# Optimization experiments

Hardware: AMD Instinct MI355X
Metric: run time of the kernel (lower is better)

The kernel has to match this reference:

```python
import jax, jax.numpy as jnp
import numpy as np

B, L, T, F, H, O = 4096, 50, 64, 3, 20, 16

def setup_inputs() -> dict:
    key = jax.random.key(0)
    ks = jax.random.split(key, 20)
    p = lambda k, s: jax.random.normal(k, s, jnp.float32) * 0.1
    inp = {
        'x': jax.random.normal(ks[0], (B, L, T, F), jnp.float32),
        'lengths': jax.random.randint(ks[1], (B, L), 0, T, jnp.int32),
        # LSTMCell params (torch gate order i,f,g,o)
        'w_ih': p(ks[2], (4 * H, F)), 'w_hh': p(ks[3], (4 * H, H)),
        'b_ih': p(ks[4], (4 * H,)), 'b_hh': p(ks[5], (4 * H,)),
        # layer-summary Linear(20,16)
        'w_lin': p(ks[6], (O, H)), 'b_lin': p(ks[7], (O,)),
        # ClassifyNet convs
        'c1_w': p(ks[8], (32, 16, 5)), 'c1_b': p(ks[9], (32,)),
        'c2_w': p(ks[10], (32, 32, 4)), 'c2_b': p(ks[11], (32,)),
        'c3_w': p(ks[12], (32, 32, 4)), 'c3_b': p(ks[13], (32,)),
        'fc1_w': p(ks[14], (16, 32 * 19)), 'fc1_b': p(ks[15], (16,)),
        'fc2_w': p(ks[16], (4, 16)), 'fc2_b': p(ks[17], (4,)),
    }
    return inp

def _conv1d(x, w, b, stride):
    y = jax.lax.conv_general_dilated(x, w, (stride,), 'VALID',
                                     dimension_numbers=('NCH', 'OIH', 'NCH'))
    return y + b[None, :, None]

def _lstm_last_h(xseq, lens, w_ih, w_hh, b_ih, b_hh):
    # xseq: [N,T,F] padded; lens: [N]. Masked batched LSTM, returns h at step len-1.
    N = xseq.shape[0]
    xT = jnp.swapaxes(xseq, 0, 1)  # [T,N,F]
    h0 = jnp.zeros((N, H), xseq.dtype)
    def step(carry, inp):
        h, c = carry
        x_t, t = inp
        gates = x_t @ w_ih.T + b_ih + h @ w_hh.T + b_hh
        i, f, g, o = jnp.split(gates, 4, axis=-1)
        c_new = jax.nn.sigmoid(f) * c + jax.nn.sigmoid(i) * jnp.tanh(g)
        h_new = jax.nn.sigmoid(o) * jnp.tanh(c_new)
        m = (t < lens)[:, None]
        return (jnp.where(m, h_new, h), jnp.where(m, c_new, c)), None
    (h, _), _ = jax.lax.scan(step, (h0, h0), (xT, jnp.arange(xT.shape[0])))
    return h

def reference(x, lengths, w_ih, w_hh, b_ih, b_hh, w_lin, b_lin,
              c1_w, c1_b, c2_w, c2_b, c3_w, c3_b, fc1_w, fc1_b, fc2_w, fc2_b):
    N = B * L
    xf = x.reshape(N, T, F)
    lens = lengths.reshape(N)
    h = _lstm_last_h(xf, lens, w_ih, w_hh, b_ih, b_hh)          # [N,20]
    summ = jax.nn.sigmoid(h @ w_lin.T + b_lin)                   # [N,16]
    summ = jnp.where((lens > 0)[:, None], summ, 0.0)             # empty layer -> zeros
    feat = jnp.swapaxes(summ.reshape(B, L, O), 1, 2)             # [B,16,50]
    y = jax.nn.relu(_conv1d(feat, c1_w, c1_b, 1))                # [B,32,46]
    y = jax.nn.relu(_conv1d(y, c2_w, c2_b, 2))                   # [B,32,22]
    y = jax.nn.relu(_conv1d(y, c3_w, c3_b, 1))                   # [B,32,19]
    y = y.reshape(B, 32 * 19)
    y = jax.nn.relu(y @ fc1_w.T + fc1_b)
    return y @ fc2_w.T + fc2_b                                   # [B,4]
```

## Files before the change

kernel.cpp:

```cpp
#include <hip/hip_runtime.h>
#include <cstdint>
#include <cstddef>

#define NB 4096
#define NL 50
#define NT 64
#define NF 3
#define NH 20
#define NO 16
#define NN (NB*NL)
#define SB 16
#define WPB 2
#define TS 16
#define HSTR 20
#define XSTR 8

typedef __attribute__((ext_vector_type(8))) short bf16x8;
typedef __attribute__((ext_vector_type(4))) float f32x4;
typedef uint2 u2a __attribute__((may_alias));
typedef uint4 u4a __attribute__((may_alias));

#if defined(__has_builtin)
#  if __has_builtin(__builtin_amdgcn_exp2f)
#    define EXP2(x) __builtin_amdgcn_exp2f(x)
#  endif
#endif
#ifndef EXP2
extern "C" __device__ float __ocml_exp2_f32(float);
#  define EXP2(x) __ocml_exp2_f32(x)
#endif

__device__ __forceinline__ float fsig(float z) {
    return __builtin_amdgcn_rcpf(1.0f + __expf(-z));
}
__device__ __forceinline__ unsigned short f2bf(float f) {
    unsigned int x = __float_as_uint(f);
    x = (x + 0x7fffu + ((x >> 16) & 1u)) >> 16;
    return (unsigned short)x;
}
__device__ __forceinline__ float bf2f(unsigned short u) {
    return __uint_as_float(((unsigned int)u) << 16);
}
__device__ __forceinline__ unsigned int cvtpk(float a, float b) {
    unsigned int r;
    asm("v_cvt_pk_bf16_f32 %0, %1, %2" : "=v"(r) : "v"(a), "v"(b));
    return r;
}

__global__ __launch_bounds__(256) void hist_kernel(const int* __restrict__ lengths,
                                                   int* __restrict__ hist) {
    __shared__ int lh[64];
    int tid = threadIdx.x;
    if (tid < 64) lh[tid] = 0;
    __syncthreads();
    int n = blockIdx.x * 256 + tid;
    if (n < NN) {
        int len = lengths[n];
        len = len < 0 ? 0 : (len > 63 ? 63 : len);
        atomicAdd(&lh[len], 1);
    }
    __syncthreads();
    if (tid < 64 && lh[tid] != 0) atomicAdd(&hist[tid], lh[tid]);
}

__global__ __launch_bounds__(128) void prep_kernel(
    const int*   __restrict__ hist,
    int*         __restrict__ cursor,
    const float* __restrict__ w_hh,
    const float* __restrict__ b_ih,
    const float* __restrict__ b_hh,
    const float* __restrict__ w_ih,
    unsigned int* __restrict__ wfrag)
{
    int tid = threadIdx.x;
    if (tid < 64) {
        int l = tid;
        int v = hist[l];
        int s = v;
#pragma unroll
        for (int d = 1; d < 64; d <<= 1) {
            int o = __shfl_up(s, d);
            if (l >= d) s += o;
        }
        cursor[l] = s - v;
    } else {
        int l = tid - 64;
        int m = l & 15, kg = l >> 4;
        for (int T = 0; T < 5; ++T) {
            int g = (m & 3) * 20 + T * 4 + (m >> 2);
            int jt = g / 20;
            float sc = (jt == 2) ? 2.8853900817779268f : -1.4426950408889634f;
            unsigned int hi[4], lo[4];
            for (int d = 0; d < 4; ++d) {
                unsigned int hw[2], lw[2];
                for (int e = 0; e < 2; ++e) {
                    int k = kg * 8 + d * 2 + e;
                    float v = 0.0f;
                    if (k < 20)       v = w_hh[g * 20 + k];
                    else if (k <= 22) v = w_ih[g * 3 + (k - 20)];
                    else if (k == 23) v = b_ih[g] + b_hh[g];
                    else if (k <= 26) v = w_ih[g * 3 + (k - 24)];
                    v *= sc;
                    unsigned short h16 = f2bf(v);
                    float r = v - bf2f(h16);
                    hw[e] = h16; lw[e] = f2bf(r);
                }
                hi[d] = hw[0] | (hw[1] << 16);
                lo[d] = lw[0] | (lw[1] << 16);
            }
            for (int d = 0; d < 4; ++d) {
                wfrag[(size_t)((T * 2 + 0) * 64 + l) * 4 + d] = hi[d];
                wfrag[(size_t)((T * 2 + 1) * 64 + l) * 4 + d] = lo[d];
            }
        }
    }
}

__global__ __launch_bounds__(256) void scatter_kernel(const int* __restrict__ lengths,
                                                      int* __restrict__ cursor,
                                                      int* __restrict__ order,
                                                      int* __restrict__ len_s) {
    __shared__ int lcnt[64];
    __shared__ int lbase[64];
    int tid = threadIdx.x;
    if (tid < 64) lcnt[tid] = 0;
    __syncthreads();
    int n = blockIdx.x * 256 + tid;
    int len = 0, myrank = 0;
    if (n < NN) {
        len = lengths[n];
        len = len < 0 ? 0 : (len > 63 ? 63 : len);
        myrank = atomicAdd(&lcnt[len], 1);
    }
    __syncthreads();
    if (tid < 64 && lcnt[tid] != 0) lbase[tid] = atomicAdd(&cursor[tid], lcnt[tid]);
    __syncthreads();
    if (n < NN) {
        int pos = lbase[len] + myrank;
        order[pos] = n;
        len_s[pos] = len;
    }
}

#define LSTM_STEP(K, MASKED)                                                     \
    {                                                                            \
        uint2 ra_ = *(const u2a*)(p1 + (K) * st1);                               \
        uint2 rb_ = *(const u2a*)(p2 + (K) * st2);                               \
        union { uint4 u; bf16x8 v; } bb_;                                        \
        bb_.u = make_uint4(ra_.x, ra_.y, rb_.x, rb_.y);                          \
        f32x4 acc[5];                                                            \
        _Pragma("unroll")                                                        \
        for (int T = 0; T < 5; ++T) {                                            \
            f32x4 z4 = {0.f, 0.f, 0.f, 0.f};                                     \
            z4     = __builtin_amdgcn_mfma_f32_16x16x32_bf16(wf[2*T],   bb_.v, z4, 0, 0, 0); \
            acc[T] = __builtin_amdgcn_mfma_f32_16x16x32_bf16(wf[2*T+1], bb_.v, z4, 0, 0, 0); \
        }                                                                        \
        bool m_ = true;                                                          \
        if (MASKED) m_ = (t0 + (K)) < mylen;                                     \
        _Pragma("unroll")                                                        \
        for (int T = 0; T < 5; ++T) {                                            \
            float Ei = EXP2(acc[T][0]);                            \
            float Ef = EXP2(acc[T][1]);                            \
            float G  = EXP2(acc[T][2]);                           \
            float Eo = EXP2(acc[T][3]);                            \
            float Ai = 1.0f + Ei, Af = 1.0f + Ef, Bg = 1.0f + G;                 \
            float t1 = Ai * Bg;                                                  \
            float num = fmaf(G - 1.0f, Af, c5[T] * t1);                          \
            float cn  = num * __builtin_amdgcn_rcpf(t1 * Af);                    \
            float ce2 = fminf(cn * 2.8853900817779268f, 43.3f);                  \
            float Ec  = EXP2(ce2);                         \
            float hn  = (Ec - 1.0f) *                                            \
                        __builtin_amdgcn_rcpf((1.0f + Eo) * (1.0f + Ec));        \
        unsigned int hp_ = cvtpk(hn, hn);                                        \
        if (m_) {                                                                \
            c5[T] = cn;                                                          \
            hbf[wid][hoff + T * 4] = (unsigned short)hp_;                        \
        }                                                                        \
        }                                                                        \
    }

__global__ __launch_bounds__(128) void lstm_kernel(
    const float* __restrict__ x,
    const int*   __restrict__ len_s,
    const int*   __restrict__ order,
    const unsigned int* __restrict__ wfrag,
    const float* __restrict__ w_lin,
    const float* __restrict__ b_lin,
    float* __restrict__ feat)
{
    __shared__ __align__(16) unsigned short hbf[WPB][SB * HSTR];
    __shared__ __align__(16) unsigned short xbf[WPB][TS * SB * XSTR];
    __shared__ __align__(16) unsigned short zbuf[WPB][8];

    const int tid  = threadIdx.x;
    const int wid  = __builtin_amdgcn_readfirstlane(tid >> 6);
    const int lane = tid & 63;
    const int n16  = lane & 15;
    const int kg   = lane >> 4;
    const int base = ((gridDim.x - 1 - blockIdx.x) * WPB + wid) * SB;

    const int mylen   = len_s[base + n16];
    const int wavemin = len_s[base];
    const int wavemax = len_s[base + SB - 1];

    for (int i = lane; i < SB * HSTR; i += 64) hbf[wid][i] = 0;
    if (lane < 8) zbuf[wid][lane] = 0;

    bf16x8 wf[10];
#pragma unroll
    for (int p = 0; p < 10; ++p) {
        union { uint4 i; bf16x8 v; } cv;
        cv.i = ((const uint4*)wfrag)[p * 64 + lane];
        wf[p] = cv.v;
    }

    int nown = order[base + n16];
    const int ssl = lane >> 2;
    const int tq  = lane & 3;
    int nsl = __shfl(nown, ssl);
    const size_t gbase = (size_t)nsl * (NT * NF) + (size_t)tq * 12;

    const unsigned short* hpw = &hbf[wid][n16 * HSTR];
    const unsigned short* p1 = (kg < 3) ? (hpw + kg * 8)
                                        : &xbf[wid][n16 * XSTR + 4];
    const unsigned short* p2 = (kg < 2) ? (hpw + kg * 8 + 4)
                             : (kg == 2 ? &xbf[wid][n16 * XSTR]
                                        : &zbuf[wid][0]);
    const int st1 = (kg == 3) ? SB * XSTR : 0;
    const int st2 = (kg == 2) ? SB * XSTR : 0;
    const int hoff = n16 * HSTR + kg;

    float c5[5];
#pragma unroll
    for (int j = 0; j < 5; ++j) c5[j] = 0.0f;

    if (wavemax > 0) {
        float4 vf[3];
#pragma unroll
        for (int j = 0; j < 3; ++j) vf[j] = *(const float4*)(x + gbase + 4 * j);

        for (int t0 = 0; t0 < wavemax; t0 += TS) {
            float f12[12] = {vf[0].x, vf[0].y, vf[0].z, vf[0].w,
                             vf[1].x, vf[1].y, vf[1].z, vf[1].w,
                             vf[2].x, vf[2].y, vf[2].z, vf[2].w};
#pragma unroll
            for (int jj = 0; jj < 4; ++jj) {
                float a0 = f12[3 * jj], a1 = f12[3 * jj + 1], a2 = f12[3 * jj + 2];
                unsigned int w0 = cvtpk(a0, a1);
                unsigned int w1 = cvtpk(a2, 1.0f);
                float r0 = a0 - __uint_as_float(w0 << 16);
                float r1 = a1 - __uint_as_float(w0 & 0xFFFF0000u);
                float r2 = a2 - __uint_as_float(w1 << 16);
                unsigned int w2 = cvtpk(r0, r1);
                unsigned int w3 = cvtpk(r2, 0.0f);
                int t = tq * 4 + jj;
                *(u4a*)&xbf[wid][(t * SB + ssl) * XSTR] = make_uint4(w0, w1, w2, w3);
            }
            if (t0 + TS < wavemax) {
                size_t off = (size_t)(t0 + TS) * NF;
#pragma unroll
                for (int j = 0; j < 3; ++j)
                    vf[j] = *(const float4*)(x + gbase + off + 4 * j);
            }

            int kmax = wavemax - t0; if (kmax > TS) kmax = TS;
            int ku = wavemin - t0;
            ku = ku < 0 ? 0 : (ku > kmax ? kmax : ku);
            int k = 0;
            for (; k < ku; ++k)   LSTM_STEP(k, false)
            for (; k < kmax; ++k) LSTM_STEP(k, true)
        }
    }

    float hl[NH];
#pragma unroll
    for (int u = 0; u < NH; ++u) hl[u] = bf2f(hbf[wid][n16 * HSTR + u]);
    float4 res;
    if (mylen > 0) {
        float r4[4];
#pragma unroll
        for (int j = 0; j < 4; ++j) {
            int o = 4 * kg + j;
            float aa = b_lin[o];
#pragma unroll
            for (int kk = 0; kk < NH; ++kk) aa += w_lin[o * NH + kk] * hl[kk];
            r4[j] = fsig(aa);
        }
        res = make_float4(r4[0], r4[1], r4[2], r4[3]);
    } else {
        res = make_float4(0.f, 0.f, 0.f, 0.f);
    }
    *(float4*)(feat + (size_t)nown * NO + 4 * kg) = res;
}

__global__ __launch_bounds__(256) void head_kernel(
    const float* __restrict__ feat,
    const float* __restrict__ c1w, const float* __restrict__ c1b,
    const float* __restrict__ c2w, const float* __restrict__ c2b,
    const float* __restrict__ c3w, const float* __restrict__ c3b,
    const float* __restrict__ f1w, const float* __restrict__ f1b,
    const float* __restrict__ f2w, const float* __restrict__ f2b,
    float* __restrict__ out)
{
    const int b0  = blockIdx.x * 2;
    const int tid = threadIdx.x;
    const int p   = tid & 63;
    const int q   = __builtin_amdgcn_readfirstlane(tid >> 6);
    const int half = p >> 5;
    const int pp   = p & 31;

    __shared__ float sf[2][16 * 50];
    __shared__ float y1[2][32 * 46];
    __shared__ float y2[2][32 * 22];
    __shared__ __align__(16) float y3[2][32 * 19];
    __shared__ float r1[2][16];

    for (int i = tid; i < 2 * NL * NO; i += 256) {
        int bb = (i >= NL * NO) ? 1 : 0;
        int j = i - bb * (NL * NO);
        int l = j >> 4, o = j & 15;
        sf[bb][o * 50 + l] = feat[(size_t)(b0 + bb) * (NL * NO) + j];
    }
    __syncthreads();

    const int oc0 = q * 8;

#pragma unroll
    for (int bb = 0; bb < 2; ++bb) {
        if (p < 46) {
            float acc[8];
#pragma unroll
            for (int oc = 0; oc < 8; ++oc) acc[oc] = c1b[oc0 + oc];
#pragma unroll
            for (int ic = 0; ic < 16; ++ic) {
#pragma unroll
                for (int tap = 0; tap < 5; ++tap) {
                    float fv = sf[bb][ic * 50 + p + tap];
#pragma unroll
                    for (int oc = 0; oc < 8; ++oc)
                        acc[oc] += c1w[((oc0 + oc) * 16 + ic) * 5 + tap] * fv;
                }
            }
#pragma unroll
            for (int oc = 0; oc < 8; ++oc)
                y1[bb][(oc0 + oc) * 46 + p] = fmaxf(acc[oc], 0.0f);
        }
    }
    __syncthreads();

    if (pp < 22) {
        float acc[8];
#pragma unroll
        for (int oc = 0; oc < 8; ++oc) acc[oc] = c2b[oc0 + oc];
#pragma unroll
        for (int ic = 0; ic < 32; ++ic) {
#pragma unroll
            for (int tap = 0; tap < 4; ++tap) {
                float fv = y1[half][ic * 46 + 2 * pp + tap];
#pragma unroll
                for (int oc = 0; oc < 8; ++oc)
                    acc[oc] += c2w[((oc0 + oc) * 32 + ic) * 4 + tap] * fv;
            }
        }
#pragma unroll
        for (int oc = 0; oc < 8; ++oc)
            y2[half][(oc0 + oc) * 22 + pp] = fmaxf(acc[oc], 0.0f);
    }
    __syncthreads();

    if (pp < 19) {
        float acc[8];
#pragma unroll
        for (int oc = 0; oc < 8; ++oc) acc[oc] = c3b[oc0 + oc];
#pragma unroll
        for (int ic = 0; ic < 32; ++ic) {
#pragma unroll
            for (int tap = 0; tap < 4; ++tap) {
                float fv = y2[half][ic * 22 + pp + tap];
#pragma unroll
                for (int oc = 0; oc < 8; ++oc)
                    acc[oc] += c3w[((oc0 + oc) * 32 + ic) * 4 + tap] * fv;
            }
        }
#pragma unroll
        for (int oc = 0; oc < 8; ++oc)
            y3[half][(oc0 + oc) * 19 + pp] = fmaxf(acc[oc], 0.0f);
    }
    __syncthreads();

    if (q < 2) {
        int u  = p & 15;
        int qq = p >> 4;
        const float4* wv = (const float4*)(f1w + u * 608 + qq * 152);
        const float4* yv = (const float4*)(&y3[q][qq * 152]);
        float acc = 0.0f;
#pragma unroll 2
        for (int k = 0; k < 38; ++k) {
            float4 a = wv[k], bv = yv[k];
            acc += a.x * bv.x + a.y * bv.y + a.z * bv.z + a.w * bv.w;
        }
        acc += __shfl_xor(acc, 16);
        acc += __shfl_xor(acc, 32);
        if (p < 16) r1[q][p] = fmaxf(acc + f1b[p], 0.0f);
    }
    __syncthreads();

    if (q < 2 && p < 4) {
        float s = f2b[p];
#pragma unroll
        for (int k = 0; k < 16; ++k) s += f2w[p * 16 + k] * r1[q][k];
        out[(size_t)(b0 + q) * 4 + p] = s;
    }
}

extern "C" void kernel_launch(void* const* d_in, const int* in_sizes, int n_in,
                              void* d_out, int out_size, void* d_ws, size_t ws_size,
                              hipStream_t stream)
{
    const float* x     = (const float*)d_in[0];
    const int*  lengths= (const int*)  d_in[1];
    const float* w_ih  = (const float*)d_in[2];
    const float* w_hh  = (const float*)d_in[3];
    const float* b_ih  = (const float*)d_in[4];
    const float* b_hh  = (const float*)d_in[5];
    const float* w_lin = (const float*)d_in[6];
    const float* b_lin = (const float*)d_in[7];
    const float* c1w   = (const float*)d_in[8];
    const float* c1b   = (const float*)d_in[9];
    const float* c2w   = (const float*)d_in[10];
    const float* c2b   = (const float*)d_in[11];
    const float* c3w   = (const float*)d_in[12];
    const float* c3b   = (const float*)d_in[13];
    const float* f1w   = (const float*)d_in[14];
    const float* f1b   = (const float*)d_in[15];
    const float* f2w   = (const float*)d_in[16];
    const float* f2b   = (const float*)d_in[17];
    float* out = (float*)d_out;

    char* ws      = (char*)d_ws;
    float* feat   = (float*)ws;
    int*   order  = (int*)(feat + (size_t)NN * NO);
    int*   len_s  = order + NN;
    int*   hist   = len_s + NN;
    int*   cursor = hist + 64;
    unsigned int* wfrag = (unsigned int*)(cursor + 64);

    hipMemsetAsync(hist, 0, 64 * sizeof(int), stream);
    hist_kernel   <<<NN / 256, 256, 0, stream>>>(lengths, hist);
    prep_kernel   <<<1, 128, 0, stream>>>(hist, cursor, w_hh, b_ih, b_hh, w_ih, wfrag);
    scatter_kernel<<<NN / 256, 256, 0, stream>>>(lengths, cursor, order, len_s);
    lstm_kernel   <<<NN / (SB * WPB), 128, 0, stream>>>(x, len_s, order, wfrag,
                                                        w_lin, b_lin, feat);
    head_kernel   <<<NB / 2, 256, 0, stream>>>(feat, c1w, c1b, c2w, c2b, c3w, c3b,
                                               f1w, f1b, f2w, f2b, out);
}
```

Baseline: 458.7 us.

## Replace global-atomic counting sort with per-chunk histograms and offsets

The counting sort of sequences by length now uses 64 fixed chunks. Each block writes its own 64-bin histogram, and the prep kernel computes a per-chunk exclusive prefix across chunks. This removes the memset and the global atomics on a 64-entry cursor that 800 blocks used to contend on. In exchange only 64 blocks run the hist and scatter passes, so those passes have much less parallelism. The order within each length bucket also changes, since positions now come from shared atomics inside a chunk of 3200 elements.

After: 434.3 us. 1.06x faster.

```diff
diff --git a/kernel.cpp b/kernel.cpp
--- a/kernel.cpp
+++ b/kernel.cpp
@@ -14,6 +14,7 @@
 #define TS 16
 #define HSTR 20
 #define XSTR 8
+#define SCH (NN/64)
 
 typedef __attribute__((ext_vector_type(8))) short bf16x8;
 typedef __attribute__((ext_vector_type(4))) float f32x4;
@@ -47,25 +48,26 @@
     return r;
 }
 
-__global__ __launch_bounds__(256) void hist_kernel(const int* __restrict__ lengths,
-                                                   int* __restrict__ hist) {
+__global__ __launch_bounds__(256) void hist64_kernel(const int* __restrict__ lengths,
+                                                     int* __restrict__ bhist) {
     __shared__ int lh[64];
-    int tid = threadIdx.x;
+    const int tid = threadIdx.x;
+    const int b   = blockIdx.x;
     if (tid < 64) lh[tid] = 0;
     __syncthreads();
-    int n = blockIdx.x * 256 + tid;
-    if (n < NN) {
-        int len = lengths[n];
+    const int base = b * SCH;
+    for (int i = tid; i < SCH; i += 256) {
+        int len = lengths[base + i];
         len = len < 0 ? 0 : (len > 63 ? 63 : len);
         atomicAdd(&lh[len], 1);
     }
     __syncthreads();
-    if (tid < 64 && lh[tid] != 0) atomicAdd(&hist[tid], lh[tid]);
+    if (tid < 64) bhist[b * 64 + tid] = lh[tid];
 }
 
 __global__ __launch_bounds__(128) void prep_kernel(
-    const int*   __restrict__ hist,
-    int*         __restrict__ cursor,
+    const int*   __restrict__ bhist,
+    int*         __restrict__ boff,
     const float* __restrict__ w_hh,
     const float* __restrict__ b_ih,
     const float* __restrict__ b_hh,
@@ -75,14 +77,21 @@
     int tid = threadIdx.x;
     if (tid < 64) {
         int l = tid;
-        int v = hist[l];
-        int s = v;
+        int tot = 0;
+#pragma unroll 8
+        for (int b = 0; b < 64; ++b) tot += bhist[b * 64 + l];
+        int s = tot;
 #pragma unroll
         for (int d = 1; d < 64; d <<= 1) {
             int o = __shfl_up(s, d);
             if (l >= d) s += o;
         }
-        cursor[l] = s - v;
+        int run = s - tot;
+#pragma unroll 8
+        for (int b = 0; b < 64; ++b) {
+            boff[b * 64 + l] = run;
+            run += bhist[b * 64 + l];
+        }
     } else {
         int l = tid - 64;
         int m = l & 15, kg = l >> 4;
@@ -116,27 +125,25 @@
     }
 }
 
-__global__ __launch_bounds__(256) void scatter_kernel(const int* __restrict__ lengths,
-                                                      int* __restrict__ cursor,
-                                                      int* __restrict__ order,
-                                                      int* __restrict__ len_s) {
+__global__ __launch_bounds__(256) void scatter64_kernel(
+    const int* __restrict__ lengths,
+    const int* __restrict__ boff,
+    int* __restrict__ order,
+    int* __restrict__ len_s)
+{
     __shared__ int lcnt[64];
     __shared__ int lbase[64];
-    int tid = threadIdx.x;
-    if (tid < 64) lcnt[tid] = 0;
-    __syncthreads();
-    int n = blockIdx.x * 256 + tid;
-    int len = 0, myrank = 0;
-    if (n < NN) {
-        len = lengths[n];
+    const int tid = threadIdx.x;
+    const int b   = blockIdx.x;
+    if (tid < 64) { lcnt[tid] = 0; lbase[tid] = boff[b * 64 + tid]; }
+    __syncthreads();
+    const int base = b * SCH;
+    for (int i = tid; i < SCH; i += 256) {
+        int n = base + i;
+        int len = lengths[n];
         len = len < 0 ? 0 : (len > 63 ? 63 : len);
-        myrank = atomicAdd(&lcnt[len], 1);
-    }
-    __syncthreads();
-    if (tid < 64 && lcnt[tid] != 0) lbase[tid] = atomicAdd(&cursor[tid], lcnt[tid]);
-    __syncthreads();
-    if (n < NN) {
-        int pos = lbase[len] + myrank;
+        int r = atomicAdd(&lcnt[len], 1);
+        int pos = lbase[len] + r;
         order[pos] = n;
         len_s[pos] = len;
     }
@@ -441,16 +448,15 @@
     float* feat   = (float*)ws;
     int*   order  = (int*)(feat + (size_t)NN * NO);
     int*   len_s  = order + NN;
-    int*   hist   = len_s + NN;
-    int*   cursor = hist + 64;
-    unsigned int* wfrag = (unsigned int*)(cursor + 64);
-
-    hipMemsetAsync(hist, 0, 64 * sizeof(int), stream);
-    hist_kernel   <<<NN / 256, 256, 0, stream>>>(lengths, hist);
-    prep_kernel   <<<1, 128, 0, stream>>>(hist, cursor, w_hh, b_ih, b_hh, w_ih, wfrag);
-    scatter_kernel<<<NN / 256, 256, 0, stream>>>(lengths, cursor, order, len_s);
-    lstm_kernel   <<<NN / (SB * WPB), 128, 0, stream>>>(x, len_s, order, wfrag,
-                                                        w_lin, b_lin, feat);
-    head_kernel   <<<NB / 2, 256, 0, stream>>>(feat, c1w, c1b, c2w, c2b, c3w, c3b,
-                                               f1w, f1b, f2w, f2b, out);
-}
+    int*   bhist  = len_s + NN;
+    int*   boff   = bhist + 64 * 64;
+    unsigned int* wfrag = (unsigned int*)(boff + 64 * 64);
+
+    hist64_kernel  <<<64, 256, 0, stream>>>(lengths, bhist);
+    prep_kernel    <<<1, 128, 0, stream>>>(bhist, boff, w_hh, b_ih, b_hh, w_ih, wfrag);
+    scatter64_kernel<<<64, 256, 0, stream>>>(lengths, boff, order, len_s);
+    lstm_kernel    <<<NN / (SB * WPB), 128, 0, stream>>>(x, len_s, order, wfrag,
+                                                         w_lin, b_lin, feat);
+    head_kernel    <<<NB / 2, 256, 0, stream>>>(feat, c1w, c1b, c2w, c2b, c3w, c3b,
+                                                f1w, f1b, f2w, f2b, out);
+}
```
